# Performance work log

Hardware: AMD Instinct MI355X
Metric: run time of the kernel (lower is better)

Reference implementation:

```python
import jax, jax.numpy as jnp
import numpy as np

N_NODES = 20000
N_EDGES = 320000
IN_DIM = 256
HIDDEN = 256
OUT_DIM = 128
N_LAYERS = 3
N_GROUPS = 4
EXP_PER_GROUP = 2
N_EXPERTS = N_GROUPS * EXP_PER_GROUP
TOP_K = 2


def setup_inputs() -> dict:
    key = jax.random.key(0)
    ks = jax.random.split(key, 12)
    d = HIDDEN
    r = 2 * d  # router/expert input dim: concat(node, neighbor-mean)
    x = jax.random.normal(ks[0], (N_NODES, IN_DIM), dtype=jnp.float32)
    edge_index = jax.random.randint(ks[1], (2, N_EDGES), 0, N_NODES, dtype=jnp.int32)
    s = 0.05
    Wg = jax.random.normal(ks[2], (N_LAYERS, r, N_GROUPS), dtype=jnp.float32) * s
    We = jax.random.normal(ks[3], (N_LAYERS, r, N_EXPERTS), dtype=jnp.float32) * s
    Ww = jax.random.normal(ks[4], (N_LAYERS, r, d), dtype=jnp.float32) * s
    W1 = jax.random.normal(ks[5], (N_LAYERS, N_EXPERTS, r, d), dtype=jnp.float32) * s
    b1 = jnp.zeros((N_LAYERS, N_EXPERTS, d), dtype=jnp.float32)
    W2 = jax.random.normal(ks[6], (N_LAYERS, N_EXPERTS, d, d), dtype=jnp.float32) * s
    b2 = jnp.zeros((N_LAYERS, N_EXPERTS, d), dtype=jnp.float32)
    wc = jax.random.normal(ks[7], (N_LAYERS, r, 1), dtype=jnp.float32) * s
    Wout = jax.random.normal(ks[8], (d, OUT_DIM), dtype=jnp.float32) * s
    return {"x": x, "edge_index": edge_index, "Wg": Wg, "We": We, "Ww": Ww,
            "W1": W1, "b1": b1, "W2": W2, "b2": b2, "wc": wc, "Wout": Wout}


def _moe_layer(h, src, dst, deg, Wg, We, Ww, W1, b1, W2, b2, wc):
    N = h.shape[0]
    # graph message passing: mean aggregation over incoming edges
    agg = jax.ops.segment_sum(h[src], dst, num_segments=N) / deg  # [N, d]
    r = jnp.concatenate([h, agg], axis=-1)  # [N, 2d] combined router input
    # hierarchical routing: group softmax x within-group expert softmax
    gp = jax.nn.softmax(r @ Wg, axis=-1)                                # [N, G]
    ep = jax.nn.softmax((r @ We).reshape(N, N_GROUPS, EXP_PER_GROUP), axis=-1)
    probs = (gp[..., None] * ep).reshape(N, N_EXPERTS)                  # [N, E]
    # top-k gating, renormalized
    topv, topi = jax.lax.top_k(probs, TOP_K)
    gates = jnp.zeros_like(probs).at[jnp.arange(N)[:, None], topi].set(topv)
    gates = gates / (gates.sum(-1, keepdims=True) + 1e-9)              # [N, E]
    # strong experts: per-expert 2-layer MLP, combined by gates
    hid = jax.nn.relu(jnp.einsum('nf,efd->ned', r, W1) + b1[None])      # [N, E, d]
    exp_out = jnp.einsum('ned,edo->neo', hid, W2) + b2[None]            # [N, E, d]
    strong = jnp.einsum('ne,neo->no', gates, exp_out)                   # [N, d]
    # weak shared expert + confidence gate blend
    weak = r @ Ww                                                       # [N, d]
    conf = jax.nn.sigmoid(r @ wc)                                       # [N, 1]
    return jax.nn.relu(conf * strong + (1.0 - conf) * weak)


def reference(x, edge_index, Wg, We, Ww, W1, b1, W2, b2, wc, Wout):
    src, dst = edge_index[0], edge_index[1]
    N = x.shape[0]
    deg = jax.ops.segment_sum(jnp.ones((edge_index.shape[1],), jnp.float32), dst,
                              num_segments=N)
    deg = jnp.maximum(deg, 1.0)[:, None]
    h = x
    for l in range(Wg.shape[0]):  # small fixed layer loop
        h = _moe_layer(h, src, dst, deg, Wg[l], We[l], Ww[l],
                       W1[l], b1[l], W2[l], b2[l], wc[l])
    return h @ Wout
```

## Files before the change

### kernel.cpp

```cpp
#include <hip/hip_runtime.h>

#define NN 20000
#define NEDGE 320000
#define D 256
#define RD 512
#define OD 128
#define NEXP 8
#define NSLOT (2*NN)
#define NODE_BLOCKS 79
#define ASSIGN_BLOCKS 157

#define LDK 40
#define PL (128 * LDK)

typedef unsigned short u16;
typedef __attribute__((ext_vector_type(8))) short short8v;
typedef __attribute__((ext_vector_type(16))) float f32x16;

__device__ __forceinline__ void split1(float v, u16& h, u16& m, u16& l) {
    unsigned b = __float_as_uint(v);
    h = (u16)(b >> 16);
    float fh = __uint_as_float(b & 0xffff0000u);
    float r1 = v - fh;
    unsigned b1 = __float_as_uint(r1);
    m = (u16)(b1 >> 16);
    float fm = __uint_as_float(b1 & 0xffff0000u);
    float r2 = r1 - fm;
    l = (u16)(__float_as_uint(r2) >> 16);
}

__device__ __forceinline__ void split8(const float4& x, const float4& y,
                                       short8v& h, short8v& m, short8v& l) {
    float v[8] = {x.x, x.y, x.z, x.w, y.x, y.y, y.z, y.w};
#pragma unroll
    for (int i = 0; i < 8; i++) {
        u16 hh, mm, ll;
        split1(v[i], hh, mm, ll);
        h[i] = (short)hh; m[i] = (short)mm; l[i] = (short)ll;
    }
}


__global__ void copy_x_zero_cnt_k(const float* __restrict__ x, float* __restrict__ r,
                                  int* __restrict__ cnt) {
    int gid = blockIdx.x * 256 + threadIdx.x;
    int n = gid >> 6;
    int c4 = gid & 63;
    if (gid < NN * (D / 4)) {
        float4 v = reinterpret_cast<const float4*>(x)[gid];
        reinterpret_cast<float4*>(r + (size_t)n * RD)[c4] = v;
    }
    if (gid < NN) cnt[gid] = 0;
}

__global__ void count_edges_k(const int* __restrict__ dst, int* __restrict__ cnt) {
    int e = blockIdx.x * 256 + threadIdx.x;
    if (e < NEDGE) atomicAdd(&cnt[dst[e]], 1);
}

__global__ void block_sums_k(const int* __restrict__ cnt, int* __restrict__ bsum) {
    __shared__ int s[256];
    int i = blockIdx.x * 256 + threadIdx.x;
    s[threadIdx.x] = (i < NN) ? cnt[i] : 0;
    __syncthreads();
    for (int off = 128; off > 0; off >>= 1) {
        if (threadIdx.x < off) s[threadIdx.x] += s[threadIdx.x + off];
        __syncthreads();
    }
    if (threadIdx.x == 0) bsum[blockIdx.x] = s[0];
}

__global__ void scan_bsums_k(int* __restrict__ bsum, int* __restrict__ row_start) {
    if (blockIdx.x == 0 && threadIdx.x == 0) {
        int acc = 0;
        for (int i = 0; i < NODE_BLOCKS; i++) { int t = bsum[i]; bsum[i] = acc; acc += t; }
        row_start[NN] = acc;
    }
}

__global__ void block_scan_k(const int* __restrict__ cnt, const int* __restrict__ bsum,
                             int* __restrict__ row_start, int* __restrict__ cur) {
    __shared__ int s[256];
    int i = blockIdx.x * 256 + threadIdx.x;
    int v = (i < NN) ? cnt[i] : 0;
    s[threadIdx.x] = v;
    __syncthreads();
    for (int off = 1; off < 256; off <<= 1) {
        int t = (threadIdx.x >= off) ? s[threadIdx.x - off] : 0;
        __syncthreads();
        s[threadIdx.x] += t;
        __syncthreads();
    }
    int excl = s[threadIdx.x] - v + bsum[blockIdx.x];
    if (i < NN) { row_start[i] = excl; cur[i] = excl; }
}

__global__ void fill_csr_k(const int* __restrict__ src, const int* __restrict__ dst,
                           int* __restrict__ cur, int* __restrict__ csr_src) {
    int e = blockIdx.x * 256 + threadIdx.x;
    if (e < NEDGE) {
        int pos = atomicAdd(&cur[dst[e]], 1);
        csr_src[pos] = src[e];
    }
}

__global__ void aggregate_k(float* __restrict__ r, const int* __restrict__ row_start,
                            const int* __restrict__ csr_src, int* __restrict__ ec) {
    if (blockIdx.x == 0 && threadIdx.x < 16) ec[threadIdx.x] = 0;
    int wid = blockIdx.x * 4 + (threadIdx.x >> 6);
    int lane = threadIdx.x & 63;
    if (wid >= NN) return;
    int beg = row_start[wid], end = row_start[wid + 1];
    float ax = 0.f, ay = 0.f, az = 0.f, aw = 0.f;
    for (int j = beg; j < end; j++) {
        int s = csr_src[j];
        float4 v = reinterpret_cast<const float4*>(r + (size_t)s * RD)[lane];
        ax += v.x; ay += v.y; az += v.z; aw += v.w;
    }
    float deg = (float)((end - beg) > 1 ? (end - beg) : 1);
    float4 o = make_float4(ax / deg, ay / deg, az / deg, aw / deg);
    reinterpret_cast<float4*>(r + (size_t)wid * RD + D)[lane] = o;
}

__global__ void router_k(const float* __restrict__ r, const float* __restrict__ Wg,
                         const float* __restrict__ We, const float* __restrict__ wc,
                         int* __restrict__ node_top, float* __restrict__ node_gate,
                         float* __restrict__ conf) {
    int wid = blockIdx.x * 4 + (threadIdx.x >> 6);
    int lane = threadIdx.x & 63;
    if (wid >= NN) return;

    const float* rrow = r + (size_t)wid * RD;
    float pg[4] = {0, 0, 0, 0};
    float pe[8] = {0, 0, 0, 0, 0, 0, 0, 0};
    float pc = 0.f;
#pragma unroll
    for (int i = 0; i < 8; i++) {
        int k = lane + i * 64;
        float rv = rrow[k];
        float4 wg = *reinterpret_cast<const float4*>(Wg + (size_t)k * 4);
        pg[0] = fmaf(rv, wg.x, pg[0]); pg[1] = fmaf(rv, wg.y, pg[1]);
        pg[2] = fmaf(rv, wg.z, pg[2]); pg[3] = fmaf(rv, wg.w, pg[3]);
        float4 w0 = *reinterpret_cast<const float4*>(We + (size_t)k * 8);
        float4 w1 = *reinterpret_cast<const float4*>(We + (size_t)k * 8 + 4);
        pe[0] = fmaf(rv, w0.x, pe[0]); pe[1] = fmaf(rv, w0.y, pe[1]);
        pe[2] = fmaf(rv, w0.z, pe[2]); pe[3] = fmaf(rv, w0.w, pe[3]);
        pe[4] = fmaf(rv, w1.x, pe[4]); pe[5] = fmaf(rv, w1.y, pe[5]);
        pe[6] = fmaf(rv, w1.z, pe[6]); pe[7] = fmaf(rv, w1.w, pe[7]);
        pc = fmaf(rv, wc[k], pc);
    }
#pragma unroll
    for (int off = 32; off > 0; off >>= 1) {
#pragma unroll
        for (int g = 0; g < 4; g++) pg[g] += __shfl_xor(pg[g], off);
#pragma unroll
        for (int g = 0; g < 8; g++) pe[g] += __shfl_xor(pe[g], off);
        pc += __shfl_xor(pc, off);
    }

    if (lane == 0) {
        float m = fmaxf(fmaxf(pg[0], pg[1]), fmaxf(pg[2], pg[3]));
        float eg[4]; float sg = 0.f;
#pragma unroll
        for (int g = 0; g < 4; g++) { eg[g] = expf(pg[g] - m); sg += eg[g]; }
        float probs[8];
#pragma unroll
        for (int g = 0; g < 4; g++) {
            float a = pe[2 * g], b = pe[2 * g + 1];
            float mm = fmaxf(a, b);
            float ea = expf(a - mm), eb = expf(b - mm);
            float inv = 1.f / (ea + eb);
            float gp = eg[g] / sg;
            probs[2 * g]     = gp * ea * inv;
            probs[2 * g + 1] = gp * eb * inv;
        }
        int i0 = 0; float v0 = probs[0];
#pragma unroll
        for (int j = 1; j < 8; j++) if (probs[j] > v0) { v0 = probs[j]; i0 = j; }
        int i1 = -1; float v1 = -1e30f;
#pragma unroll
        for (int j = 0; j < 8; j++) if (j != i0 && probs[j] > v1) { v1 = probs[j]; i1 = j; }
        float s = v0 + v1 + 1e-9f;
        node_top[2 * wid] = i0;  node_top[2 * wid + 1] = i1;
        node_gate[2 * wid] = v0 / s;  node_gate[2 * wid + 1] = v1 / s;
        conf[wid] = 1.f / (1.f + expf(-pc));
    }
}

__global__ void expert_hist_k(const int* __restrict__ node_top, int* __restrict__ ec) {
    __shared__ int h[NEXP];
    if (threadIdx.x < NEXP) h[threadIdx.x] = 0;
    __syncthreads();
    int i = blockIdx.x * 256 + threadIdx.x;
    if (i < NSLOT) atomicAdd(&h[node_top[i]], 1);
    __syncthreads();
    if (threadIdx.x < NEXP && h[threadIdx.x] > 0) atomicAdd(&ec[threadIdx.x], h[threadIdx.x]);
}

__global__ void expert_scan_k(const int* __restrict__ ec, int* __restrict__ es,
                              int* __restrict__ ecur) {
    if (blockIdx.x == 0 && threadIdx.x == 0) {
        int acc = 0;
        for (int e = 0; e < NEXP; e++) { es[e] = acc; acc += ec[e]; ecur[e] = 0; }
        es[NEXP] = acc;
    }
}

__global__ void fill_experts_k(const int* __restrict__ node_top, const float* __restrict__ node_gate,
                               const int* __restrict__ es, int* __restrict__ ecur,
                               int* __restrict__ slot_node, float* __restrict__ slot_gate,
                               int* __restrict__ node_slot) {
    __shared__ int hcnt[NEXP], hbase[NEXP];
    int tid = threadIdx.x;
    if (tid < NEXP) hcnt[tid] = 0;
    __syncthreads();
    int i = blockIdx.x * 256 + tid;
    int e = 0, local = 0;
    bool act = (i < NSLOT);
    if (act) {
        e = node_top[i];
        local = atomicAdd(&hcnt[e], 1);
    }
    __syncthreads();
    if (tid < NEXP) hbase[tid] = (hcnt[tid] > 0) ? atomicAdd(&ecur[tid], hcnt[tid]) : 0;
    __syncthreads();
    if (act) {
        int slot = es[e] + hbase[e] + local;
        slot_node[slot] = i >> 1;
        slot_gate[slot] = node_gate[i];
        node_slot[i] = slot;
    }
}

__global__ void combine_k(const float* __restrict__ expout, const float* __restrict__ weak,
                          const float* __restrict__ conf, const int* __restrict__ node_slot,
                          float* __restrict__ r) {
    int gid = blockIdx.x * 256 + threadIdx.x;
    if (gid >= NN * (D / 4)) return;
    int n = gid >> 6, c4 = gid & 63;
    int s0 = node_slot[2 * n], s1 = node_slot[2 * n + 1];
    float4 e0 = reinterpret_cast<const float4*>(expout + (size_t)s0 * D)[c4];
    float4 e1 = reinterpret_cast<const float4*>(expout + (size_t)s1 * D)[c4];
    float4 w  = reinterpret_cast<const float4*>(weak + (size_t)n * D)[c4];
    float cf = conf[n], cg = 1.f - cf;
    float4 o;
    o.x = fmaxf(cf * (e0.x + e1.x) + cg * w.x, 0.f);
    o.y = fmaxf(cf * (e0.y + e1.y) + cg * w.y, 0.f);
    o.z = fmaxf(cf * (e0.z + e1.z) + cg * w.z, 0.f);
    o.w = fmaxf(cf * (e0.w + e1.w) + cg * w.w, 0.f);
    reinterpret_cast<float4*>(r + (size_t)n * RD)[c4] = o;
}

__global__ void tsplit_k(const float* __restrict__ src, u16* __restrict__ dH,
                         u16* __restrict__ dM, u16* __restrict__ dL, int K, int N) {
    __shared__ float t[64][65];
    int mat = blockIdx.z;
    int k0 = blockIdx.x * 64, n0 = blockIdx.y * 64;
    const float* s = src + (size_t)mat * K * N;
#pragma unroll
    for (int i = 0; i < 16; i++) {
        int idx = threadIdx.x + i * 256;
        int kk = idx >> 6, nn = idx & 63;
        t[kk][nn] = s[(size_t)(k0 + kk) * N + n0 + nn];
    }
    __syncthreads();
    size_t base = (size_t)mat * N * K;
#pragma unroll
    for (int i = 0; i < 16; i++) {
        int idx = threadIdx.x + i * 256;
        int nn = idx >> 6, kk = idx & 63;
        float v = t[kk][nn];
        u16 h, m, l; split1(v, h, m, l);
        size_t o = base + (size_t)(n0 + nn) * K + k0 + kk;
        dH[o] = h; dM[o] = m; dL[o] = l;
    }
}

template <int MODE>
__global__ __launch_bounds__(256, 2) void gemm_mfma(
    const float* __restrict__ A, int lda,
    const u16* __restrict__ BH, const u16* __restrict__ BM,
    const u16* __restrict__ BL,
    const float* __restrict__ bias,
    float* __restrict__ C, int ldc,
    const int* __restrict__ es,
    const int* __restrict__ slot_node,
    const float* __restrict__ slot_gate,
    int M, int N, int K) {
    __shared__ u16 sA[3 * PL];
    __shared__ u16 sB[3 * PL];

    int tid = threadIdx.x;
    int row0, valid_rows;
    if (MODE == 0) {
        row0 = blockIdx.x * 128;
        valid_rows = M - row0; if (valid_rows > 128) valid_rows = 128;
    } else {
        int bx = blockIdx.x, acc0 = 0, expert = -1, mt = 0;
        row0 = 0; valid_rows = 0;
        for (int e = 0; e < NEXP; e++) {
            int c = es[e + 1] - es[e];
            int t = (c + 127) >> 7;
            if (bx < acc0 + t) {
                expert = e; mt = bx - acc0; row0 = es[e] + (mt << 7);
                valid_rows = c - (mt << 7); if (valid_rows > 128) valid_rows = 128;
                break;
            }
            acc0 += t;
        }
        if (expert < 0) return;
        size_t bo = (size_t)expert * N * K;
        BH += bo; BM += bo; BL += bo;
        bias += expert * D;
    }
    int ncol0 = blockIdx.y * 128;

    int sr = tid >> 2;
    int ksf = (tid & 3) * 8;

    int g0, g1;
    {
        int i0 = row0 + sr, i1 = i0 + 64;
        if (MODE == 1) {
            i0 = i0 < NSLOT ? i0 : NSLOT - 1;
            i1 = i1 < NSLOT ? i1 : NSLOT - 1;
            g0 = slot_node[i0]; g1 = slot_node[i1];
        } else {
            int cap = M - 1;
            g0 = i0 < M ? i0 : cap;
            g1 = i1 < M ? i1 : cap;
        }
    }
    const float* pA0 = A + (size_t)g0 * lda + ksf;
    const float* pA1 = A + (size_t)g1 * lda + ksf;
    size_t bro0 = (size_t)(ncol0 + sr) * K + ksf;
    size_t bro1 = bro0 + (size_t)64 * K;

    int lane = tid & 63;
    int wr = ((tid >> 7) & 1) * 64;
    int wc = ((tid >> 6) & 1) * 64;
    int fl = lane & 31;
    int fh8 = (lane >> 5) * 8;

    f32x16 acc[2][2] = {};

    int aoff = sr * LDK + ksf;

    for (int kt = 0; kt < K; kt += 32) {
        float4 a00 = *reinterpret_cast<const float4*>(pA0 + kt);
        float4 a01 = *reinterpret_cast<const float4*>(pA0 + kt + 4);
        float4 a10 = *reinterpret_cast<const float4*>(pA1 + kt);
        float4 a11 = *reinterpret_cast<const float4*>(pA1 + kt + 4);
        short8v b0h = *reinterpret_cast<const short8v*>(BH + bro0 + kt);
        short8v b0m = *reinterpret_cast<const short8v*>(BM + bro0 + kt);
        short8v b0l = *reinterpret_cast<const short8v*>(BL + bro0 + kt);
        short8v b1h = *reinterpret_cast<const short8v*>(BH + bro1 + kt);
        short8v b1m = *reinterpret_cast<const short8v*>(BM + bro1 + kt);
        short8v b1l = *reinterpret_cast<const short8v*>(BL + bro1 + kt);
        __syncthreads();
        {
            short8v h, m, l;
            split8(a00, a01, h, m, l);
            *reinterpret_cast<short8v*>(&sA[0 * PL + aoff]) = h;
            *reinterpret_cast<short8v*>(&sA[1 * PL + aoff]) = m;
            *reinterpret_cast<short8v*>(&sA[2 * PL + aoff]) = l;
            split8(a10, a11, h, m, l);
            *reinterpret_cast<short8v*>(&sA[0 * PL + aoff + 64 * LDK]) = h;
            *reinterpret_cast<short8v*>(&sA[1 * PL + aoff + 64 * LDK]) = m;
            *reinterpret_cast<short8v*>(&sA[2 * PL + aoff + 64 * LDK]) = l;
            *reinterpret_cast<short8v*>(&sB[0 * PL + aoff]) = b0h;
            *reinterpret_cast<short8v*>(&sB[1 * PL + aoff]) = b0m;
            *reinterpret_cast<short8v*>(&sB[2 * PL + aoff]) = b0l;
            *reinterpret_cast<short8v*>(&sB[0 * PL + aoff + 64 * LDK]) = b1h;
            *reinterpret_cast<short8v*>(&sB[1 * PL + aoff + 64 * LDK]) = b1m;
            *reinterpret_cast<short8v*>(&sB[2 * PL + aoff + 64 * LDK]) = b1l;
        }
        __syncthreads();
#pragma unroll
        for (int kk = 0; kk < 2; kk++) {
            int ko = kk * 16 + fh8;
            const u16* A0 = sA + (wr + fl) * LDK + ko;
            const u16* A1 = A0 + 32 * LDK;
            const u16* B0 = sB + (wc + fl) * LDK + ko;
            const u16* B1 = B0 + 32 * LDK;
            short8v aH0 = *reinterpret_cast<const short8v*>(A0);
            short8v aM0 = *reinterpret_cast<const short8v*>(A0 + PL);
            short8v aL0 = *reinterpret_cast<const short8v*>(A0 + 2 * PL);
            short8v aH1 = *reinterpret_cast<const short8v*>(A1);
            short8v aM1 = *reinterpret_cast<const short8v*>(A1 + PL);
            short8v aL1 = *reinterpret_cast<const short8v*>(A1 + 2 * PL);
            short8v bH0 = *reinterpret_cast<const short8v*>(B0);
            short8v bM0 = *reinterpret_cast<const short8v*>(B0 + PL);
            short8v bL0 = *reinterpret_cast<const short8v*>(B0 + 2 * PL);
            short8v bH1 = *reinterpret_cast<const short8v*>(B1);
            short8v bM1 = *reinterpret_cast<const short8v*>(B1 + PL);
            short8v bL1 = *reinterpret_cast<const short8v*>(B1 + 2 * PL);
#define MFMA_ACC(d, a, b) d = __builtin_amdgcn_mfma_f32_32x32x16_bf16(a, b, d, 0, 0, 0)
            MFMA_ACC(acc[0][0], aH0, bH0); MFMA_ACC(acc[0][0], aH0, bM0);
            MFMA_ACC(acc[0][0], aM0, bH0); MFMA_ACC(acc[0][0], aH0, bL0);
            MFMA_ACC(acc[0][0], aM0, bM0); MFMA_ACC(acc[0][0], aL0, bH0);
            MFMA_ACC(acc[0][1], aH0, bH1); MFMA_ACC(acc[0][1], aH0, bM1);
            MFMA_ACC(acc[0][1], aM0, bH1); MFMA_ACC(acc[0][1], aH0, bL1);
            MFMA_ACC(acc[0][1], aM0, bM1); MFMA_ACC(acc[0][1], aL0, bH1);
            MFMA_ACC(acc[1][0], aH1, bH0); MFMA_ACC(acc[1][0], aH1, bM0);
            MFMA_ACC(acc[1][0], aM1, bH0); MFMA_ACC(acc[1][0], aH1, bL0);
            MFMA_ACC(acc[1][0], aM1, bM0); MFMA_ACC(acc[1][0], aL1, bH0);
            MFMA_ACC(acc[1][1], aH1, bH1); MFMA_ACC(acc[1][1], aH1, bM1);
            MFMA_ACC(acc[1][1], aM1, bH1); MFMA_ACC(acc[1][1], aH1, bL1);
            MFMA_ACC(acc[1][1], aM1, bM1); MFMA_ACC(acc[1][1], aL1, bH1);
#undef MFMA_ACC
        }
    }

    int fh = lane >> 5;
#pragma unroll
    for (int i = 0; i < 2; i++) {
#pragma unroll
        for (int j = 0; j < 2; j++) {
            int colg = ncol0 + wc + j * 32 + fl;
            float bv = (MODE != 0) ? bias[colg] : 0.f;
#pragma unroll
            for (int rg = 0; rg < 16; rg++) {
                int lrow = wr + i * 32 + (rg & 3) + 8 * (rg >> 2) + 4 * fh;
                if (lrow >= valid_rows) continue;
                int grow = row0 + lrow;
                float v = acc[i][j][rg] + bv;
                if (MODE == 1) {
                    v = fmaxf(v, 0.f);
                } else if (MODE == 2) {
                    v *= slot_gate[grow];
                }
                C[(size_t)grow * ldc + colg] = v;
            }
        }
    }
}

extern "C" void kernel_launch(void* const* d_in, const int* in_sizes, int n_in,
                              void* d_out, int out_size, void* d_ws, size_t ws_size,
                              hipStream_t stream) {
    (void)in_sizes; (void)n_in; (void)out_size; (void)ws_size;
    const float* x    = (const float*)d_in[0];
    const int*   ei   = (const int*)d_in[1];
    const float* Wg   = (const float*)d_in[2];
    const float* We   = (const float*)d_in[3];
    const float* Ww   = (const float*)d_in[4];
    const float* W1   = (const float*)d_in[5];
    const float* b1   = (const float*)d_in[6];
    const float* W2   = (const float*)d_in[7];
    const float* b2   = (const float*)d_in[8];
    const float* wcp  = (const float*)d_in[9];
    const float* Wout = (const float*)d_in[10];
    float* out = (float*)d_out;

    char* p = (char*)d_ws;
    auto alloc = [&](size_t bytes) -> char* {
        char* q = p; p += (bytes + 255) & ~(size_t)255; return q;
    };
    int*   cnt       = (int*)alloc((size_t)NN * 4);
    int*   row_start = (int*)alloc((size_t)(NN + 1) * 4);
    int*   cur       = (int*)alloc((size_t)NN * 4);
    int*   bsum      = (int*)alloc(128 * 4);
    int*   csr_src   = (int*)alloc((size_t)NEDGE * 4);
    float* r         = (float*)alloc((size_t)NN * RD * 4);
    float* hid       = (float*)alloc((size_t)NSLOT * D * 4);
    float* expout    = (float*)alloc((size_t)NSLOT * D * 4);
    float* conf      = (float*)alloc((size_t)NN * 4);
    int*   node_top  = (int*)alloc((size_t)2 * NN * 4);
    float* node_gate = (float*)alloc((size_t)2 * NN * 4);
    int*   node_slot = (int*)alloc((size_t)2 * NN * 4);
    int*   slot_node = (int*)alloc((size_t)NSLOT * 4);
    float* slot_gate = (float*)alloc((size_t)NSLOT * 4);
    int*   ec        = (int*)alloc(64 * 4);
    int*   es        = (int*)alloc(64 * 4);
    int*   ecur      = (int*)alloc(64 * 4);
    u16* w1tH = (u16*)alloc((size_t)NEXP * D * RD * 2);
    u16* w1tM = (u16*)alloc((size_t)NEXP * D * RD * 2);
    u16* w1tL = (u16*)alloc((size_t)NEXP * D * RD * 2);
    u16* w2tH = (u16*)alloc((size_t)NEXP * D * D * 2);
    u16* w2tM = (u16*)alloc((size_t)NEXP * D * D * 2);
    u16* w2tL = (u16*)alloc((size_t)NEXP * D * D * 2);
    u16* wwtH = (u16*)alloc((size_t)D * RD * 2);
    u16* wwtM = (u16*)alloc((size_t)D * RD * 2);
    u16* wwtL = (u16*)alloc((size_t)D * RD * 2);
    u16* wotH = (u16*)alloc((size_t)OD * D * 2);
    u16* wotM = (u16*)alloc((size_t)OD * D * 2);
    u16* wotL = (u16*)alloc((size_t)OD * D * 2);
    float* weak = hid;

    const int* srcp = ei;
    const int* dstp = ei + NEDGE;
    const int EB = (NEDGE + 255) / 256;

    copy_x_zero_cnt_k<<<5000, 256, 0, stream>>>(x, r, cnt);
    count_edges_k<<<EB, 256, 0, stream>>>(dstp, cnt);
    block_sums_k<<<NODE_BLOCKS, 256, 0, stream>>>(cnt, bsum);
    scan_bsums_k<<<1, 64, 0, stream>>>(bsum, row_start);
    block_scan_k<<<NODE_BLOCKS, 256, 0, stream>>>(cnt, bsum, row_start, cur);
    fill_csr_k<<<EB, 256, 0, stream>>>(srcp, dstp, cur, csr_src);
    tsplit_k<<<dim3(4, 2, 1), 256, 0, stream>>>(Wout, wotH, wotM, wotL, D, OD);

    for (int l = 0; l < 3; l++) {
        tsplit_k<<<dim3(8, 4, 8), 256, 0, stream>>>(W1 + (size_t)l * NEXP * RD * D,
                                                    w1tH, w1tM, w1tL, RD, D);
        tsplit_k<<<dim3(4, 4, 8), 256, 0, stream>>>(W2 + (size_t)l * NEXP * D * D,
                                                    w2tH, w2tM, w2tL, D, D);
        tsplit_k<<<dim3(8, 4, 1), 256, 0, stream>>>(Ww + (size_t)l * RD * D,
                                                    wwtH, wwtM, wwtL, RD, D);
        aggregate_k<<<5000, 256, 0, stream>>>(r, row_start, csr_src, ec);
        router_k<<<5000, 256, 0, stream>>>(r,
            Wg + (size_t)l * RD * 4, We + (size_t)l * RD * 8, wcp + (size_t)l * RD,
            node_top, node_gate, conf);
        expert_hist_k<<<ASSIGN_BLOCKS, 256, 0, stream>>>(node_top, ec);
        expert_scan_k<<<1, 64, 0, stream>>>(ec, es, ecur);
        fill_experts_k<<<ASSIGN_BLOCKS, 256, 0, stream>>>(node_top, node_gate, es, ecur,
                                                          slot_node, slot_gate, node_slot);
        gemm_mfma<1><<<dim3(320, 2), 256, 0, stream>>>(r, RD, w1tH, w1tM, w1tL,
            b1 + (size_t)l * NEXP * D, hid, D, es, slot_node, slot_gate, NSLOT, D, RD);
        gemm_mfma<2><<<dim3(320, 2), 256, 0, stream>>>(hid, D, w2tH, w2tM, w2tL,
            b2 + (size_t)l * NEXP * D, expout, D, es, slot_node, slot_gate, NSLOT, D, D);
        gemm_mfma<0><<<dim3(157, 2), 256, 0, stream>>>(r, RD, wwtH, wwtM, wwtL,
            nullptr, weak, D, nullptr, nullptr, nullptr, NN, D, RD);
        combine_k<<<5000, 256, 0, stream>>>(expout, weak, conf, node_slot, r);
    }
    gemm_mfma<0><<<dim3(157, 1), 256, 0, stream>>>(r, RD, wotH, wotM, wotL,
        nullptr, out, OD, nullptr, nullptr, nullptr, NN, OD, D);
}
```

Baseline: 958.6 us.

## Pre-tile B weights into MFMA fragment order and load directly to registers

Weight conversion now writes the bf16 hi/mid/lo splits in a fragment-major tiled layout matching the MFMA B operand. The GEMM then loads B fragments straight from global memory into registers, skipping the shared-memory stage for B. Shared memory now holds only the A tile, with the K step reduced from 32 to 16 and occupancy raised to 3 blocks per CU. The trade is twice as many barriers per K, in exchange for less LDS traffic and footprint.

```diff
diff --git a/kernel.cpp b/kernel.cpp
--- a/kernel.cpp
+++ b/kernel.cpp
@@ -9,9 +9,6 @@
 #define NSLOT (2*NN)
 #define NODE_BLOCKS 79
 #define ASSIGN_BLOCKS 157
-
-#define LDK 40
-#define PL (128 * LDK)
 
 typedef unsigned short u16;
 typedef __attribute__((ext_vector_type(8))) short short8v;
@@ -251,33 +248,37 @@
     reinterpret_cast<float4*>(r + (size_t)n * RD)[c4] = o;
 }
 
-__global__ void tsplit_k(const float* __restrict__ src, u16* __restrict__ dH,
-                         u16* __restrict__ dM, u16* __restrict__ dL, int K, int N) {
-    __shared__ float t[64][65];
-    int mat = blockIdx.z;
-    int k0 = blockIdx.x * 64, n0 = blockIdx.y * 64;
-    const float* s = src + (size_t)mat * K * N;
-#pragma unroll
-    for (int i = 0; i < 16; i++) {
-        int idx = threadIdx.x + i * 256;
-        int kk = idx >> 6, nn = idx & 63;
-        t[kk][nn] = s[(size_t)(k0 + kk) * N + n0 + nn];
-    }
-    __syncthreads();
-    size_t base = (size_t)mat * N * K;
-#pragma unroll
-    for (int i = 0; i < 16; i++) {
-        int idx = threadIdx.x + i * 256;
-        int nn = idx >> 6, kk = idx & 63;
-        float v = t[kk][nn];
-        u16 h, m, l; split1(v, h, m, l);
-        size_t o = base + (size_t)(n0 + nn) * K + k0 + kk;
-        dH[o] = h; dM[o] = m; dL[o] = l;
-    }
+__global__ void btile_k(const float* __restrict__ src, u16* __restrict__ dH,
+                        u16* __restrict__ dM, u16* __restrict__ dL,
+                        int K, int N, int total) {
+    int gid = blockIdx.x * 256 + threadIdx.x;
+    if (gid >= total) return;
+    int l = gid & 63;
+    int tile = gid >> 6;
+    int K16 = K >> 4;
+    int kb = tile % K16;
+    int t2 = tile / K16;
+    int N32 = N >> 5;
+    int nb = t2 % N32;
+    int mat = t2 / N32;
+    int kbase = (kb << 4) + ((l >> 5) << 3);
+    int n = (nb << 5) + (l & 31);
+    const float* s = src + ((size_t)mat * K + kbase) * N + n;
+    short8v vh, vm, vl;
+#pragma unroll
+    for (int j = 0; j < 8; j++) {
+        u16 hh, mm, ll;
+        split1(s[(size_t)j * N], hh, mm, ll);
+        vh[j] = (short)hh; vm[j] = (short)mm; vl[j] = (short)ll;
+    }
+    size_t o = (size_t)gid * 8;
+    *reinterpret_cast<short8v*>(dH + o) = vh;
+    *reinterpret_cast<short8v*>(dM + o) = vm;
+    *reinterpret_cast<short8v*>(dL + o) = vl;
 }
 
 template <int MODE>
-__global__ __launch_bounds__(256, 2) void gemm_mfma(
+__global__ __launch_bounds__(256, 3) void gemm_mfma(
     const float* __restrict__ A, int lda,
     const u16* __restrict__ BH, const u16* __restrict__ BM,
     const u16* __restrict__ BL,
@@ -287,8 +288,9 @@
     const int* __restrict__ slot_node,
     const float* __restrict__ slot_gate,
     int M, int N, int K) {
-    __shared__ u16 sA[3 * PL];
-    __shared__ u16 sB[3 * PL];
+    constexpr int LDK2 = 24;
+    constexpr int PL2 = 128 * LDK2;
+    __shared__ u16 sA[3 * PL2];
 
     int tid = threadIdx.x;
     int row0, valid_rows;
@@ -315,101 +317,75 @@
     }
     int ncol0 = blockIdx.y * 128;
 
-    int sr = tid >> 2;
-    int ksf = (tid & 3) * 8;
-
-    int g0, g1;
+    int srow = tid >> 1;
+    int koff = (tid & 1) * 8;
+    int grow;
     {
-        int i0 = row0 + sr, i1 = i0 + 64;
+        int i0 = row0 + srow;
         if (MODE == 1) {
             i0 = i0 < NSLOT ? i0 : NSLOT - 1;
-            i1 = i1 < NSLOT ? i1 : NSLOT - 1;
-            g0 = slot_node[i0]; g1 = slot_node[i1];
+            grow = slot_node[i0];
         } else {
-            int cap = M - 1;
-            g0 = i0 < M ? i0 : cap;
-            g1 = i1 < M ? i1 : cap;
+            grow = i0 < M ? i0 : M - 1;
         }
     }
-    const float* pA0 = A + (size_t)g0 * lda + ksf;
-    const float* pA1 = A + (size_t)g1 * lda + ksf;
-    size_t bro0 = (size_t)(ncol0 + sr) * K + ksf;
-    size_t bro1 = bro0 + (size_t)64 * K;
+    const float* pA = A + (size_t)grow * lda + koff;
 
     int lane = tid & 63;
     int wr = ((tid >> 7) & 1) * 64;
     int wc = ((tid >> 6) & 1) * 64;
     int fl = lane & 31;
     int fh8 = (lane >> 5) * 8;
+    int K16 = K >> 4;
+    int nb0 = (ncol0 + wc) >> 5;
+    size_t tb0 = ((size_t)nb0 * K16) * 512 + (size_t)lane * 8;
+    size_t tb1 = ((size_t)(nb0 + 1) * K16) * 512 + (size_t)lane * 8;
 
     f32x16 acc[2][2] = {};
-
-    int aoff = sr * LDK + ksf;
-
-    for (int kt = 0; kt < K; kt += 32) {
-        float4 a00 = *reinterpret_cast<const float4*>(pA0 + kt);
-        float4 a01 = *reinterpret_cast<const float4*>(pA0 + kt + 4);
-        float4 a10 = *reinterpret_cast<const float4*>(pA1 + kt);
-        float4 a11 = *reinterpret_cast<const float4*>(pA1 + kt + 4);
-        short8v b0h = *reinterpret_cast<const short8v*>(BH + bro0 + kt);
-        short8v b0m = *reinterpret_cast<const short8v*>(BM + bro0 + kt);
-        short8v b0l = *reinterpret_cast<const short8v*>(BL + bro0 + kt);
-        short8v b1h = *reinterpret_cast<const short8v*>(BH + bro1 + kt);
-        short8v b1m = *reinterpret_cast<const short8v*>(BM + bro1 + kt);
-        short8v b1l = *reinterpret_cast<const short8v*>(BL + bro1 + kt);
+    int aoff = srow * LDK2 + koff;
+    const u16* Af0 = sA + (wr + fl) * LDK2 + fh8;
+    const u16* Af1 = Af0 + 32 * LDK2;
+
+    for (int kt = 0; kt < K; kt += 16) {
+        float4 av0 = *reinterpret_cast<const float4*>(pA + kt);
+        float4 av1 = *reinterpret_cast<const float4*>(pA + kt + 4);
+        size_t o0 = tb0 + (size_t)(kt >> 4) * 512;
+        size_t o1 = tb1 + (size_t)(kt >> 4) * 512;
+        short8v bH0 = *reinterpret_cast<const short8v*>(BH + o0);
+        short8v bM0 = *reinterpret_cast<const short8v*>(BM + o0);
+        short8v bL0 = *reinterpret_cast<const short8v*>(BL + o0);
+        short8v bH1 = *reinterpret_cast<const short8v*>(BH + o1);
+        short8v bM1 = *reinterpret_cast<const short8v*>(BM + o1);
+        short8v bL1 = *reinterpret_cast<const short8v*>(BL + o1);
         __syncthreads();
         {
             short8v h, m, l;
-            split8(a00, a01, h, m, l);
-            *reinterpret_cast<short8v*>(&sA[0 * PL + aoff]) = h;
-            *reinterpret_cast<short8v*>(&sA[1 * PL + aoff]) = m;
-            *reinterpret_cast<short8v*>(&sA[2 * PL + aoff]) = l;
-            split8(a10, a11, h, m, l);
-            *reinterpret_cast<short8v*>(&sA[0 * PL + aoff + 64 * LDK]) = h;
-            *reinterpret_cast<short8v*>(&sA[1 * PL + aoff + 64 * LDK]) = m;
-            *reinterpret_cast<short8v*>(&sA[2 * PL + aoff + 64 * LDK]) = l;
-            *reinterpret_cast<short8v*>(&sB[0 * PL + aoff]) = b0h;
-            *reinterpret_cast<short8v*>(&sB[1 * PL + aoff]) = b0m;
-            *reinterpret_cast<short8v*>(&sB[2 * PL + aoff]) = b0l;
-            *reinterpret_cast<short8v*>(&sB[0 * PL + aoff + 64 * LDK]) = b1h;
-            *reinterpret_cast<short8v*>(&sB[1 * PL + aoff + 64 * LDK]) = b1m;
-            *reinterpret_cast<short8v*>(&sB[2 * PL + aoff + 64 * LDK]) = b1l;
+            split8(av0, av1, h, m, l);
+            *reinterpret_cast<short8v*>(&sA[0 * PL2 + aoff]) = h;
+            *reinterpret_cast<short8v*>(&sA[1 * PL2 + aoff]) = m;
+            *reinterpret_cast<short8v*>(&sA[2 * PL2 + aoff]) = l;
         }
         __syncthreads();
-#pragma unroll
-        for (int kk = 0; kk < 2; kk++) {
-            int ko = kk * 16 + fh8;
-            const u16* A0 = sA + (wr + fl) * LDK + ko;
-            const u16* A1 = A0 + 32 * LDK;
-            const u16* B0 = sB + (wc + fl) * LDK + ko;
-            const u16* B1 = B0 + 32 * LDK;
-            short8v aH0 = *reinterpret_cast<const short8v*>(A0);
-            short8v aM0 = *reinterpret_cast<const short8v*>(A0 + PL);
-            short8v aL0 = *reinterpret_cast<const short8v*>(A0 + 2 * PL);
-            short8v aH1 = *reinterpret_cast<const short8v*>(A1);
-            short8v aM1 = *reinterpret_cast<const short8v*>(A1 + PL);
-            short8v aL1 = *reinterpret_cast<const short8v*>(A1 + 2 * PL);
-            short8v bH0 = *reinterpret_cast<const short8v*>(B0);
-            short8v bM0 = *reinterpret_cast<const short8v*>(B0 + PL);
-            short8v bL0 = *reinterpret_cast<const short8v*>(B0 + 2 * PL);
-            short8v bH1 = *reinterpret_cast<const short8v*>(B1);
-            short8v bM1 = *reinterpret_cast<const short8v*>(B1 + PL);
-            short8v bL1 = *reinterpret_cast<const short8v*>(B1 + 2 * PL);
+        short8v aH0 = *reinterpret_cast<const short8v*>(Af0);
+        short8v aM0 = *reinterpret_cast<const short8v*>(Af0 + PL2);
+        short8v aL0 = *reinterpret_cast<const short8v*>(Af0 + 2 * PL2);
+        short8v aH1 = *reinterpret_cast<const short8v*>(Af1);
+        short8v aM1 = *reinterpret_cast<const short8v*>(Af1 + PL2);
+        short8v aL1 = *reinterpret_cast<const short8v*>(Af1 + 2 * PL2);
 #define MFMA_ACC(d, a, b) d = __builtin_amdgcn_mfma_f32_32x32x16_bf16(a, b, d, 0, 0, 0)
-            MFMA_ACC(acc[0][0], aH0, bH0); MFMA_ACC(acc[0][0], aH0, bM0);
-            MFMA_ACC(acc[0][0], aM0, bH0); MFMA_ACC(acc[0][0], aH0, bL0);
-            MFMA_ACC(acc[0][0], aM0, bM0); MFMA_ACC(acc[0][0], aL0, bH0);
-            MFMA_ACC(acc[0][1], aH0, bH1); MFMA_ACC(acc[0][1], aH0, bM1);
-            MFMA_ACC(acc[0][1], aM0, bH1); MFMA_ACC(acc[0][1], aH0, bL1);
-            MFMA_ACC(acc[0][1], aM0, bM1); MFMA_ACC(acc[0][1], aL0, bH1);
-            MFMA_ACC(acc[1][0], aH1, bH0); MFMA_ACC(acc[1][0], aH1, bM0);
-            MFMA_ACC(acc[1][0], aM1, bH0); MFMA_ACC(acc[1][0], aH1, bL0);
-            MFMA_ACC(acc[1][0], aM1, bM0); MFMA_ACC(acc[1][0], aL1, bH0);
-            MFMA_ACC(acc[1][1], aH1, bH1); MFMA_ACC(acc[1][1], aH1, bM1);
-            MFMA_ACC(acc[1][1], aM1, bH1); MFMA_ACC(acc[1][1], aH1, bL1);
-            MFMA_ACC(acc[1][1], aM1, bM1); MFMA_ACC(acc[1][1], aL1, bH1);
+        MFMA_ACC(acc[0][0], aH0, bH0); MFMA_ACC(acc[0][0], aH0, bM0);
+        MFMA_ACC(acc[0][0], aM0, bH0); MFMA_ACC(acc[0][0], aH0, bL0);
+        MFMA_ACC(acc[0][0], aM0, bM0); MFMA_ACC(acc[0][0], aL0, bH0);
+        MFMA_ACC(acc[0][1], aH0, bH1); MFMA_ACC(acc[0][1], aH0, bM1);
+        MFMA_ACC(acc[0][1], aM0, bH1); MFMA_ACC(acc[0][1], aH0, bL1);
+        MFMA_ACC(acc[0][1], aM0, bM1); MFMA_ACC(acc[0][1], aL0, bH1);
+        MFMA_ACC(acc[1][0], aH1, bH0); MFMA_ACC(acc[1][0], aH1, bM0);
+        MFMA_ACC(acc[1][0], aM1, bH0); MFMA_ACC(acc[1][0], aH1, bL0);
+        MFMA_ACC(acc[1][0], aM1, bM0); MFMA_ACC(acc[1][0], aL1, bH0);
+        MFMA_ACC(acc[1][1], aH1, bH1); MFMA_ACC(acc[1][1], aH1, bM1);
+        MFMA_ACC(acc[1][1], aM1, bH1); MFMA_ACC(acc[1][1], aH1, bL1);
+        MFMA_ACC(acc[1][1], aM1, bM1); MFMA_ACC(acc[1][1], aL1, bH1);
 #undef MFMA_ACC
-        }
     }
 
     int fh = lane >> 5;
@@ -423,14 +399,14 @@
             for (int rg = 0; rg < 16; rg++) {
                 int lrow = wr + i * 32 + (rg & 3) + 8 * (rg >> 2) + 4 * fh;
                 if (lrow >= valid_rows) continue;
-                int grow = row0 + lrow;
+                int growo = row0 + lrow;
                 float v = acc[i][j][rg] + bv;
                 if (MODE == 1) {
                     v = fmaxf(v, 0.f);
                 } else if (MODE == 2) {
-                    v *= slot_gate[grow];
+                    v *= slot_gate[growo];
                 }
-                C[(size_t)grow * ldc + colg] = v;
+                C[(size_t)growo * ldc + colg] = v;
             }
         }
     }
@@ -498,15 +474,15 @@
     scan_bsums_k<<<1, 64, 0, stream>>>(bsum, row_start);
     block_scan_k<<<NODE_BLOCKS, 256, 0, stream>>>(cnt, bsum, row_start, cur);
     fill_csr_k<<<EB, 256, 0, stream>>>(srcp, dstp, cur, csr_src);
-    tsplit_k<<<dim3(4, 2, 1), 256, 0, stream>>>(Wout, wotH, wotM, wotL, D, OD);
+    btile_k<<<16, 256, 0, stream>>>(Wout, wotH, wotM, wotL, D, OD, 4096);
 
     for (int l = 0; l < 3; l++) {
-        tsplit_k<<<dim3(8, 4, 8), 256, 0, stream>>>(W1 + (size_t)l * NEXP * RD * D,
-                                                    w1tH, w1tM, w1tL, RD, D);
-        tsplit_k<<<dim3(4, 4, 8), 256, 0, stream>>>(W2 + (size_t)l * NEXP * D * D,
-                                                    w2tH, w2tM, w2tL, D, D);
-        tsplit_k<<<dim3(8, 4, 1), 256, 0, stream>>>(Ww + (size_t)l * RD * D,
-                                                    wwtH, wwtM, wwtL, RD, D);
+        btile_k<<<512, 256, 0, stream>>>(W1 + (size_t)l * NEXP * RD * D,
+                                         w1tH, w1tM, w1tL, RD, D, 131072);
+        btile_k<<<256, 256, 0, stream>>>(W2 + (size_t)l * NEXP * D * D,
+                                         w2tH, w2tM, w2tL, D, D, 65536);
+        btile_k<<<64, 256, 0, stream>>>(Ww + (size_t)l * RD * D,
+                                        wwtH, wwtM, wwtL, RD, D, 16384);
         aggregate_k<<<5000, 256, 0, stream>>>(r, row_start, csr_src, ec);
         router_k<<<5000, 256, 0, stream>>>(r,
             Wg + (size_t)l * RD * 4, We + (size_t)l * RD * 8, wcp + (size_t)l * RD,
```

After: 840.8 us. 12.3% less time.
